# Performance work log

Measured on AMD Instinct MI355X. Metric: run time of the kernel, lower is better.

The kernel has to match this reference:

```python
import jax, jax.numpy as jnp
import numpy as np

B, N, D = 4, 2048, 512
H, DH = 8, 64
MLP = 2048
EPS = 1e-5


def setup_inputs() -> dict:
    key = jax.random.key(0)
    ks = jax.random.split(key, 8)
    s = lambda fan_in: 1.0 / np.sqrt(fan_in)
    return {
        "x": jax.random.normal(ks[0], (B, N, D), jnp.float32),
        "ln1_g": jnp.ones((D,), jnp.float32),
        "ln1_b": jnp.zeros((D,), jnp.float32),
        "Wqkv": jax.random.normal(ks[1], (D, 3 * H * DH), jnp.float32) * s(D),
        "temperature": jnp.asarray(np.log(DH ** -0.5), jnp.float32),
        "Wo": jax.random.normal(ks[2], (H * DH, D), jnp.float32) * s(H * DH),
        "bo": jnp.zeros((D,), jnp.float32),
        "ln2_g": jnp.ones((D,), jnp.float32),
        "ln2_b": jnp.zeros((D,), jnp.float32),
        "W1": jax.random.normal(ks[3], (D, MLP), jnp.float32) * s(D),
        "b1": jnp.zeros((MLP,), jnp.float32),
        "W2": jax.random.normal(ks[4], (MLP, D), jnp.float32) * s(MLP),
        "b2": jnp.zeros((D,), jnp.float32),
    }


def _layernorm(x, g, b):
    mu = jnp.mean(x, axis=-1, keepdims=True)
    var = jnp.var(x, axis=-1, keepdims=True)
    return (x - mu) * jax.lax.rsqrt(var + EPS) * g + b


def _lsa(x, Wqkv, temperature, Wo, bo):
    b, n, _ = x.shape
    qkv = x @ Wqkv  # [b, n, 3*H*DH]
    q, k, v = jnp.split(qkv, 3, axis=-1)
    rs = lambda t: t.reshape(b, n, H, DH).transpose(0, 2, 1, 3)  # b h n d
    q, k, v = rs(q), rs(k), rs(v)
    dots = jnp.einsum("bhnd,bhmd->bhnm", q, k) * jnp.exp(temperature)
    mask_value = -jnp.finfo(dots.dtype).max
    eye = jnp.eye(n, dtype=bool)
    dots = jnp.where(eye, mask_value, dots)  # mask diagonal (LSA)
    attn = jax.nn.softmax(dots, axis=-1)
    out = jnp.einsum("bhnm,bhmd->bhnd", attn, v)
    out = out.transpose(0, 2, 1, 3).reshape(b, n, H * DH)
    return out @ Wo + bo


def _ffn(x, W1, b1, W2, b2):
    h = jax.nn.gelu(x @ W1 + b1, approximate=False)
    return h @ W2 + b2


def reference(x, ln1_g, ln1_b, Wqkv, temperature, Wo, bo,
              ln2_g, ln2_b, W1, b1, W2, b2):
    y = _lsa(_layernorm(x, ln1_g, ln1_b), Wqkv, temperature, Wo, bo) + x
    z = _ffn(_layernorm(y, ln2_g, ln2_b), W1, b1, W2, b2) + y
    return (z, x)
```

## Files before the change

### kernel.cpp

```cpp
#include <hip/hip_runtime.h>
#include <math.h>

typedef __attribute__((ext_vector_type(4))) float f32x4;
typedef __attribute__((ext_vector_type(8))) short short8;

#define DEV __device__ __forceinline__

DEV short f2bf(float f){
  union { float f; unsigned u; } v; v.f = f;
  unsigned r = v.u + 0x7fffu + ((v.u >> 16) & 1u);
  return (short)(r >> 16);
}
DEV float bf2f(short s){
  union { unsigned u; float f; } v; v.u = ((unsigned)(unsigned short)s) << 16; return v.f;
}
DEV float exp2_hw(float x){ float r; asm("v_exp_f32 %0, %1" : "=v"(r) : "v"(x)); return r; }
DEV float rcp_hw(float x){ float r; asm("v_rcp_f32 %0, %1" : "=v"(r) : "v"(x)); return r; }
DEV unsigned cvtpk(float a, float b){
  unsigned r; asm("v_cvt_pk_bf16_f32 %0, %1, %2" : "=v"(r) : "v"(a), "v"(b)); return r;
}
DEV void gload_lds16(const short* src, short* lds){
  __builtin_amdgcn_global_load_lds(
      (const __attribute__((address_space(1))) void*)src,
      (__attribute__((address_space(3))) void*)lds, 16, 0, 0);
}

__global__ __launch_bounds__(256) void transpose_bf16_kernel(
    const float* __restrict__ W, short* __restrict__ Wt, int K, int N)
{
  __shared__ float tile[32][33];
  int nb = blockIdx.x * 32, kb = blockIdx.y * 32;
  int tx = threadIdx.x & 31, ty = threadIdx.x >> 5;
  #pragma unroll
  for (int i = ty; i < 32; i += 8)
    tile[i][tx] = W[(size_t)(kb + i) * N + nb + tx];
  __syncthreads();
  #pragma unroll
  for (int i = ty; i < 32; i += 8)
    Wt[(size_t)(nb + i) * K + kb + tx] = f2bf(tile[tx][i]);
}

template<int COPYX>
__global__ __launch_bounds__(256) void ln_kernel(
    const float* __restrict__ x, const float* __restrict__ g,
    const float* __restrict__ b, short* __restrict__ out,
    float* __restrict__ xcopy)
{
  int row  = blockIdx.x * 4 + (threadIdx.x >> 6);
  int lane = threadIdx.x & 63;
  const float* xr = x + (size_t)row * 512 + lane * 8;
  f32x4 v0 = *(const f32x4*)(xr);
  f32x4 v1 = *(const f32x4*)(xr + 4);
  float s  = (v0[0]+v0[1]+v0[2]+v0[3]) + (v1[0]+v1[1]+v1[2]+v1[3]);
  float sq = (v0[0]*v0[0]+v0[1]*v0[1]+v0[2]*v0[2]+v0[3]*v0[3])
           + (v1[0]*v1[0]+v1[1]*v1[1]+v1[2]*v1[2]+v1[3]*v1[3]);
  #pragma unroll
  for (int off = 1; off < 64; off <<= 1) {
    s  += __shfl_xor(s, off);
    sq += __shfl_xor(sq, off);
  }
  float mu  = s * (1.0f / 512.0f);
  float var = sq * (1.0f / 512.0f) - mu * mu;
  float rstd = rsqrtf(var + 1e-5f);
  f32x4 g0 = *(const f32x4*)(g + lane * 8);
  f32x4 g1 = *(const f32x4*)(g + lane * 8 + 4);
  f32x4 b0 = *(const f32x4*)(b + lane * 8);
  f32x4 b1 = *(const f32x4*)(b + lane * 8 + 4);
  float o[8];
  #pragma unroll
  for (int j = 0; j < 4; ++j) o[j]     = (v0[j] - mu) * rstd * g0[j] + b0[j];
  #pragma unroll
  for (int j = 0; j < 4; ++j) o[4 + j] = (v1[j] - mu) * rstd * g1[j] + b1[j];
  uint4 pk;
  pk.x = cvtpk(o[0], o[1]); pk.y = cvtpk(o[2], o[3]);
  pk.z = cvtpk(o[4], o[5]); pk.w = cvtpk(o[6], o[7]);
  *(uint4*)(out + (size_t)row * 512 + lane * 8) = pk;
  if (COPYX) {
    float* xc = xcopy + (size_t)row * 512 + lane * 8;
    *(f32x4*)(xc)     = v0;
    *(f32x4*)(xc + 4) = v1;
  }
}

template<int EPI, int BM, typename OutT>
__global__ __launch_bounds__(256) void gemm_bt_kernel(
    const short* __restrict__ A, const short* __restrict__ Bt,
    OutT* __restrict__ C, const float* __restrict__ bias,
    const float* __restrict__ resid, short* __restrict__ vt,
    int M, int N, int K)
{
  constexpr int MFR  = BM / 32;
  constexpr int NFR  = 4;
  constexpr int HALF = BM * 64 + 128 * 64;
  __shared__ __align__(16) short smem[2 * HALF];

  int tid = threadIdx.x;
  int lane = tid & 63, wid = tid >> 6;
  int l16 = lane & 15, lq = lane >> 4;

  int gx = gridDim.x;
  int nwg = gx * gridDim.y;
  int orig = blockIdx.y * gx + blockIdx.x;
  int swz = (orig & 7) * (nwg >> 3) + (orig >> 3);
  int bn = swz % gx, bm = swz / gx;

  int wm = wid >> 1, wn = wid & 1;

  const short* gaP[BM / 32];
  const short* gbP[4];
  #pragma unroll
  for (int i = 0; i < BM / 32; ++i) {
    int gg = i * 4 + wid;
    gaP[i] = A + (size_t)(bm * BM + (gg >> 1) * 16 + l16) * K + (gg & 1) * 32 + lq * 8;
  }
  #pragma unroll
  for (int i = 0; i < 4; ++i) {
    int gg = i * 4 + wid;
    gbP[i] = Bt + (size_t)(bn * 128 + (gg >> 1) * 16 + l16) * K + (gg & 1) * 32 + lq * 8;
  }

  auto STAGE = [&](int bufi, int k0) {
    short* As_ = smem + bufi * HALF;
    short* Bs_ = As_ + BM * 64;
    #pragma unroll
    for (int i = 0; i < BM / 32; ++i)
      gload_lds16(gaP[i] + k0, As_ + (i * 4 + wid) * 512);
    #pragma unroll
    for (int i = 0; i < 4; ++i)
      gload_lds16(gbP[i] + k0, Bs_ + (i * 4 + wid) * 512);
  };

  f32x4 acc[MFR][NFR] = {};

  STAGE(0, 0);
  asm volatile("s_waitcnt vmcnt(0)");
  __syncthreads();

  int nt = K >> 6;
  for (int t = 0; t < nt; ++t) {
    int cur = t & 1;
    if (t + 1 < nt) STAGE(cur ^ 1, (t + 1) << 6);
    const short* As_ = smem + cur * HALF;
    const short* Bs_ = As_ + BM * 64;
    #pragma unroll
    for (int kc = 0; kc < 2; ++kc) {
      short8 af[MFR], bfr[NFR];
      #pragma unroll
      for (int m = 0; m < MFR; ++m)
        af[m] = *(const short8*)(As_ + ((wm * MFR + m) * 2 + kc) * 512 + lane * 8);
      #pragma unroll
      for (int n = 0; n < NFR; ++n)
        bfr[n] = *(const short8*)(Bs_ + ((wn * NFR + n) * 2 + kc) * 512 + lane * 8);
      #pragma unroll
      for (int m = 0; m < MFR; ++m)
        #pragma unroll
        for (int n = 0; n < NFR; ++n)
          acc[m][n] = __builtin_amdgcn_mfma_f32_16x16x32_bf16(af[m], bfr[n], acc[m][n], 0, 0, 0);
    }
    __syncthreads();
  }

  if (EPI == 3 && bn >= 8) {
    short* T = smem;
    #pragma unroll
    for (int m = 0; m < MFR; ++m)
      #pragma unroll
      for (int n = 0; n < NFR; ++n) {
        int c = wn * 64 + n * 16 + l16;
        #pragma unroll
        for (int r = 0; r < 4; ++r) {
          int rowl = wm * 64 + m * 16 + lq * 4 + r;
          T[c * 128 + (rowl ^ ((c & 7) << 4))] = f2bf(acc[m][n][r]);
        }
      }
    __syncthreads();
    int b2 = bm >> 4;
    int nnb = (bm & 15) * 128;
    int tn = tid & 15;
    #pragma unroll
    for (int c8 = 0; c8 < 8; ++c8) {
      int c = c8 * 16 + (tid >> 4);
      short8 v = *(const short8*)(T + c * 128 + ((tn * 8) ^ ((c & 7) << 4)));
      if (tn & 1) {
        short8 w;
        #pragma unroll
        for (int j = 0; j < 8; ++j) w[j] = v[j ^ 4];
        v = w;
      }
      int c2 = bn * 128 + c - 1024;
      int bh = b2 * 8 + (c2 >> 6);
      int d  = c2 & 63;
      *(short8*)(vt + ((size_t)(bh * 64 + d)) * 2048 + nnb + tn * 8) = v;
    }
    return;
  }

  float bv[NFR];
  #pragma unroll
  for (int n = 0; n < NFR; ++n)
    bv[n] = (EPI == 0 || EPI == 3) ? 0.0f : bias[bn * 128 + (wn * NFR + n) * 16 + l16];

  #pragma unroll
  for (int m = 0; m < MFR; ++m) {
    #pragma unroll
    for (int r = 0; r < 4; ++r) {
      int row = bm * BM + (wm * MFR + m) * 16 + lq * 4 + r;
      #pragma unroll
      for (int n = 0; n < NFR; ++n) {
        int col = bn * 128 + (wn * NFR + n) * 16 + l16;
        float v = acc[m][n][r];
        if (EPI == 1 || EPI == 2) v += bv[n];
        if (EPI == 2) v = 0.5f * v * (1.0f + erff(v * 0.70710678f));
        if (EPI == 1) v += resid[(size_t)row * N + col];
        if constexpr (sizeof(OutT) == 2)
          ((short*)C)[(size_t)row * N + col] = f2bf(v);
        else
          ((float*)C)[(size_t)row * N + col] = v;
      }
    }
  }
}

__global__ __launch_bounds__(256, 2) void attn_kernel(
    const short* __restrict__ qkv, const short* __restrict__ vt,
    const float* __restrict__ temp_ptr, short* __restrict__ out)
{
  __shared__ __align__(16) short smem[16384];

  int tid = threadIdx.x;
  int lane = tid & 63, wid = tid >> 6;
  int l16 = lane & 15, lq = lane >> 4;
  int hi = lq >> 1, lq0 = lq & 1;

  int orig = blockIdx.y * 16 + blockIdx.x;
  int swz = (orig & 7) * 64 + (orig >> 3);
  int qb = swz & 15, bh = swz >> 4;
  int b = bh >> 3, h = bh & 7;

  const short* qbase = qkv + (size_t)b * 2048 * 1536 + h * 64;
  const short* kbase = qbase + 512;
  const short* vbase = vt + (size_t)bh * 64 * 2048;

  float scale = __expf(temp_ptr[0]) * 1.44269504f;
  int q0 = qb * 128 + wid * 32;

  short8 qfrag[2][2];
  #pragma unroll
  for (int qf = 0; qf < 2; ++qf) {
    int qrow = q0 + qf * 16 + l16;
    #pragma unroll
    for (int c = 0; c < 2; ++c) {
      short8 raw = *(const short8*)(qbase + (size_t)qrow * 1536 + c * 32 + lq * 8);
      short8 sc;
      #pragma unroll
      for (int j = 0; j < 8; ++j) sc[j] = f2bf(bf2f(raw[j]) * scale);
      qfrag[qf][c] = sc;
    }
  }

  f32x4 accO[2][4] = {};
  float l[2] = {0.f, 0.f};

  auto STAGE = [&](int bufi, int k0) {
    #pragma unroll
    for (int i = 0; i < 2; ++i) {
      int w16 = i * 256 + tid;
      int sub = w16 >> 7;
      int cc  = (w16 >> 6) & 1;
      int lq2 = (w16 >> 4) & 3;
      int l2  = w16 & 15;
      const short* srcK = kbase + (size_t)(k0 + sub * 16 + l2) * 1536 + cc * 32 + lq2 * 8;
      __builtin_amdgcn_global_load_lds(
          (const __attribute__((address_space(1))) void*)srcK,
          (__attribute__((address_space(3))) void*)((char*)smem + bufi * 8192 + (i * 4 + wid) * 1024),
          16, 0, 0);
      const short* srcV = vbase + (size_t)(sub * 16 + l2) * 2048 + k0 + cc * 32 + lq2 * 8;
      __builtin_amdgcn_global_load_lds(
          (const __attribute__((address_space(1))) void*)srcV,
          (__attribute__((address_space(3))) void*)((char*)smem + 16384 + bufi * 8192 + (i * 4 + wid) * 1024),
          16, 0, 0);
    }
  };

  STAGE(0, 0);
  asm volatile("s_waitcnt vmcnt(0)");
  __syncthreads();

  for (int k0 = 0; k0 < 2048; k0 += 64) {
    int cur = (k0 >> 6) & 1;
    if (k0 + 64 < 2048) STAGE(cur ^ 1, k0 + 64);

    const short* kls = smem + cur * 4096;
    const short* vls = smem + 8192 + cur * 4096;

    f32x4 accS[2][4] = {};
    __builtin_amdgcn_s_setprio(1);
    #pragma unroll
    for (int s = 0; s < 4; ++s) {
      short8 kf0 = *(const short8*)(kls + (s * 2 + 0) * 512 + lane * 8);
      short8 kf1 = *(const short8*)(kls + (s * 2 + 1) * 512 + lane * 8);
      #pragma unroll
      for (int qf = 0; qf < 2; ++qf) {
        accS[qf][s] = __builtin_amdgcn_mfma_f32_16x16x32_bf16(kf0, qfrag[qf][0], accS[qf][s], 0, 0, 0);
        accS[qf][s] = __builtin_amdgcn_mfma_f32_16x16x32_bf16(kf1, qfrag[qf][1], accS[qf][s], 0, 0, 0);
      }
    }
    __builtin_amdgcn_s_setprio(0);

    if ((q0 & ~63) == k0) {
      #pragma unroll
      for (int qf = 0; qf < 2; ++qf) {
        int qg = q0 + qf * 16 + l16;
        #pragma unroll
        for (int s = 0; s < 4; ++s)
          #pragma unroll
          for (int r = 0; r < 4; ++r)
            if (k0 + s * 16 + lq * 4 + r == qg) accS[qf][s][r] = -30000.f;
      }
    }

    short8 pa[2][2];
    #pragma unroll
    for (int qf = 0; qf < 2; ++qf) {
      float sum = 0.f;
      unsigned W[4][2];
      #pragma unroll
      for (int s = 0; s < 4; ++s) {
        float p0 = exp2_hw(accS[qf][s][0]);
        float p1 = exp2_hw(accS[qf][s][1]);
        float p2 = exp2_hw(accS[qf][s][2]);
        float p3 = exp2_hw(accS[qf][s][3]);
        sum += (p0 + p1) + (p2 + p3);
        W[s][0] = cvtpk(p0, p1);
        W[s][1] = cvtpk(p2, p3);
      }
      sum += __shfl_xor(sum, 16);
      sum += __shfl_xor(sum, 32);
      l[qf] += sum;

      unsigned K0[2], S0[2], K2[2], S2[2], R0[2], R2[2];
      #pragma unroll
      for (int w = 0; w < 2; ++w) {
        K0[w] = hi ? W[1][w] : W[0][w];
        S0[w] = hi ? W[0][w] : W[1][w];
        K2[w] = hi ? W[3][w] : W[2][w];
        S2[w] = hi ? W[2][w] : W[3][w];
      }
      #pragma unroll
      for (int w = 0; w < 2; ++w) {
        R0[w] = (unsigned)__shfl_xor((int)S0[w], 32);
        R2[w] = (unsigned)__shfl_xor((int)S2[w], 32);
      }
      bool sw = (hi != lq0);
      unsigned FA[2], FB[2], sA[2], sB[2], GA[2], GB[2];
      #pragma unroll
      for (int w = 0; w < 2; ++w) {
        sA[w] = sw ? K0[w] : R0[w];  FA[w] = sw ? R0[w] : K0[w];
        sB[w] = sw ? K2[w] : R2[w];  FB[w] = sw ? R2[w] : K2[w];
      }
      #pragma unroll
      for (int w = 0; w < 2; ++w) {
        GA[w] = (unsigned)__shfl_xor((int)sA[w], 16);
        GB[w] = (unsigned)__shfl_xor((int)sB[w], 16);
      }
      union { unsigned u[4]; short8 s8; } p0u, p1u;
      p0u.u[0] = FA[0]; p0u.u[1] = FA[1]; p0u.u[2] = GA[0]; p0u.u[3] = GA[1];
      p1u.u[0] = FB[0]; p1u.u[1] = FB[1]; p1u.u[2] = GB[0]; p1u.u[3] = GB[1];
      pa[qf][0] = p0u.s8;
      pa[qf][1] = p1u.s8;
    }

    short8 vfr[4][2];
    #pragma unroll
    for (int d = 0; d < 4; ++d) {
      vfr[d][0] = *(const short8*)(vls + (d * 2 + 0) * 512 + lane * 8);
      vfr[d][1] = *(const short8*)(vls + (d * 2 + 1) * 512 + lane * 8);
    }
    __builtin_amdgcn_s_setprio(1);
    #pragma unroll
    for (int qf = 0; qf < 2; ++qf)
      #pragma unroll
      for (int d = 0; d < 4; ++d) {
        accO[qf][d] = __builtin_amdgcn_mfma_f32_16x16x32_bf16(vfr[d][0], pa[qf][0], accO[qf][d], 0, 0, 0);
        accO[qf][d] = __builtin_amdgcn_mfma_f32_16x16x32_bf16(vfr[d][1], pa[qf][1], accO[qf][d], 0, 0, 0);
      }
    __builtin_amdgcn_s_setprio(0);

    __syncthreads();
  }

  #pragma unroll
  for (int qf = 0; qf < 2; ++qf) {
    float inv = rcp_hw(l[qf]);
    int qg = q0 + qf * 16 + l16;
    size_t rowoff = (size_t)(b * 2048 + qg) * 512 + h * 64;
    #pragma unroll
    for (int d = 0; d < 4; ++d) {
      unsigned w0 = cvtpk(accO[qf][d][0] * inv, accO[qf][d][1] * inv);
      unsigned w1 = cvtpk(accO[qf][d][2] * inv, accO[qf][d][3] * inv);
      uint2 pk; pk.x = w0; pk.y = w1;
      *(uint2*)(out + rowoff + d * 16 + lq * 4) = pk;
    }
  }
}

extern "C" void kernel_launch(void* const* d_in, const int* in_sizes, int n_in,
                              void* d_out, int out_size, void* d_ws, size_t ws_size,
                              hipStream_t stream)
{
  const float* x    = (const float*)d_in[0];
  const float* ln1g = (const float*)d_in[1];
  const float* ln1b = (const float*)d_in[2];
  const float* Wqkv = (const float*)d_in[3];
  const float* temp = (const float*)d_in[4];
  const float* Wo   = (const float*)d_in[5];
  const float* bo   = (const float*)d_in[6];
  const float* ln2g = (const float*)d_in[7];
  const float* ln2b = (const float*)d_in[8];
  const float* W1   = (const float*)d_in[9];
  const float* b1   = (const float*)d_in[10];
  const float* W2   = (const float*)d_in[11];
  const float* b2   = (const float*)d_in[12];
  float* out = (float*)d_out;

  char* ws = (char*)d_ws;
  short* wqkv_t = (short*)(ws);
  short* wo_t   = (short*)(ws + 1572864);
  short* w1_t   = (short*)(ws + 2097152);
  short* w2_t   = (short*)(ws + 4194304);
  short* h      = (short*)(ws + 6291456);
  short* qkv    = (short*)(ws + 14680064);
  short* attn   = (short*)(ws + 39845888);
  float* y      = (float*)(ws + 48234496);
  short* vt     = (short*)(ws + 48234496);
  short* t      = (short*)(ws + 14680064);

  const int M = 8192;

  transpose_bf16_kernel<<<dim3(1536 / 32, 512 / 32),  256, 0, stream>>>(Wqkv, wqkv_t, 512, 1536);
  transpose_bf16_kernel<<<dim3(512 / 32, 512 / 32),   256, 0, stream>>>(Wo,   wo_t,   512, 512);
  transpose_bf16_kernel<<<dim3(2048 / 32, 512 / 32),  256, 0, stream>>>(W1,   w1_t,   512, 2048);
  transpose_bf16_kernel<<<dim3(512 / 32, 2048 / 32),  256, 0, stream>>>(W2,   w2_t,   2048, 512);

  ln_kernel<1><<<M / 4, 256, 0, stream>>>(x, ln1g, ln1b, h, out + (size_t)M * 512);

  gemm_bt_kernel<3, 128, short><<<dim3(1536 / 128, M / 128), 256, 0, stream>>>(
      h, wqkv_t, qkv, nullptr, nullptr, vt, M, 1536, 512);

  attn_kernel<<<dim3(16, 32), 256, 0, stream>>>(qkv, vt, temp, attn);

  gemm_bt_kernel<1, 64, float><<<dim3(512 / 128, M / 64), 256, 0, stream>>>(
      attn, wo_t, y, bo, x, nullptr, M, 512, 512);

  ln_kernel<0><<<M / 4, 256, 0, stream>>>(y, ln2g, ln2b, h, nullptr);

  gemm_bt_kernel<2, 128, short><<<dim3(2048 / 128, M / 128), 256, 0, stream>>>(
      h, w1_t, t, b1, nullptr, nullptr, M, 2048, 512);

  gemm_bt_kernel<1, 64, float><<<dim3(512 / 128, M / 64), 256, 0, stream>>>(
      t, w2_t, out, b2, y, nullptr, M, 512, 2048);
}
```

Baseline: 232.6 us.

## Triple-buffer LDS staging in GEMM and attention with partial vmcnt waits

Both the GEMM and the attention kernel move from double-buffered LDS staging with a full vmcnt(0) wait plus two barriers per iteration to a three-stage ring buffer. Each iteration waits only on the oldest outstanding load group and issues a single barrier. The GEMM k-step also shrinks from 64 to 32, so each stage holds a smaller tile, and MFMA blocks get raised priority. The goal is to keep two global-to-LDS loads in flight and hide memory latency behind compute. In exchange the attention kernel uses more LDS, which can limit occupancy, and the hand-counted vmcnt values must match the exact number of loads issued per stage.

```diff
diff --git a/kernel.cpp b/kernel.cpp
--- a/kernel.cpp
+++ b/kernel.cpp
@@ -89,10 +89,11 @@
     const float* __restrict__ resid, short* __restrict__ vt,
     int M, int N, int K)
 {
-  constexpr int MFR  = BM / 32;
-  constexpr int NFR  = 4;
-  constexpr int HALF = BM * 64 + 128 * 64;
-  __shared__ __align__(16) short smem[2 * HALF];
+  constexpr int MFR = BM / 32;
+  constexpr int NFR = 4;
+  constexpr int AI  = BM / 64;
+  constexpr int BUF = BM * 32 + 128 * 32;
+  __shared__ __align__(16) short smem[3 * BUF];
 
   int tid = threadIdx.x;
   int lane = tid & 63, wid = tid >> 6;
@@ -106,61 +107,65 @@
 
   int wm = wid >> 1, wn = wid & 1;
 
-  const short* gaP[BM / 32];
-  const short* gbP[4];
-  #pragma unroll
-  for (int i = 0; i < BM / 32; ++i) {
+  const short* gaP[AI];
+  const short* gbP[2];
+  #pragma unroll
+  for (int i = 0; i < AI; ++i) {
     int gg = i * 4 + wid;
-    gaP[i] = A + (size_t)(bm * BM + (gg >> 1) * 16 + l16) * K + (gg & 1) * 32 + lq * 8;
-  }
-  #pragma unroll
-  for (int i = 0; i < 4; ++i) {
+    gaP[i] = A + (size_t)(bm * BM + gg * 16 + l16) * K + lq * 8;
+  }
+  #pragma unroll
+  for (int i = 0; i < 2; ++i) {
     int gg = i * 4 + wid;
-    gbP[i] = Bt + (size_t)(bn * 128 + (gg >> 1) * 16 + l16) * K + (gg & 1) * 32 + lq * 8;
+    gbP[i] = Bt + (size_t)(bn * 128 + gg * 16 + l16) * K + lq * 8;
   }
 
   auto STAGE = [&](int bufi, int k0) {
-    short* As_ = smem + bufi * HALF;
-    short* Bs_ = As_ + BM * 64;
-    #pragma unroll
-    for (int i = 0; i < BM / 32; ++i)
-      gload_lds16(gaP[i] + k0, As_ + (i * 4 + wid) * 512);
-    #pragma unroll
-    for (int i = 0; i < 4; ++i)
-      gload_lds16(gbP[i] + k0, Bs_ + (i * 4 + wid) * 512);
+    short* base = smem + bufi * BUF;
+    #pragma unroll
+    for (int i = 0; i < AI; ++i)
+      gload_lds16(gaP[i] + k0, base + (i * 4 + wid) * 512);
+    #pragma unroll
+    for (int i = 0; i < 2; ++i)
+      gload_lds16(gbP[i] + k0, base + BM * 32 + (i * 4 + wid) * 512);
   };
 
   f32x4 acc[MFR][NFR] = {};
 
   STAGE(0, 0);
-  asm volatile("s_waitcnt vmcnt(0)");
-  __syncthreads();
-
-  int nt = K >> 6;
+  STAGE(1, 32);
+
+  int nt = K >> 5;
   for (int t = 0; t < nt; ++t) {
-    int cur = t & 1;
-    if (t + 1 < nt) STAGE(cur ^ 1, (t + 1) << 6);
-    const short* As_ = smem + cur * HALF;
-    const short* Bs_ = As_ + BM * 64;
-    #pragma unroll
-    for (int kc = 0; kc < 2; ++kc) {
-      short8 af[MFR], bfr[NFR];
-      #pragma unroll
-      for (int m = 0; m < MFR; ++m)
-        af[m] = *(const short8*)(As_ + ((wm * MFR + m) * 2 + kc) * 512 + lane * 8);
+    if (t + 1 < nt) {
+      if constexpr (AI == 2) asm volatile("s_waitcnt vmcnt(4)" ::: "memory");
+      else                   asm volatile("s_waitcnt vmcnt(3)" ::: "memory");
+    } else {
+      asm volatile("s_waitcnt vmcnt(0)" ::: "memory");
+    }
+    __builtin_amdgcn_s_barrier();
+    __builtin_amdgcn_sched_barrier(0);
+    if (t + 2 < nt) STAGE((t + 2) % 3, (t + 2) << 5);
+
+    const short* base = smem + (t % 3) * BUF;
+    short8 af[MFR], bfr[NFR];
+    #pragma unroll
+    for (int m = 0; m < MFR; ++m)
+      af[m] = *(const short8*)(base + (wm * MFR + m) * 512 + lane * 8);
+    #pragma unroll
+    for (int n = 0; n < NFR; ++n)
+      bfr[n] = *(const short8*)(base + BM * 32 + (wn * NFR + n) * 512 + lane * 8);
+    __builtin_amdgcn_s_setprio(1);
+    #pragma unroll
+    for (int m = 0; m < MFR; ++m)
       #pragma unroll
       for (int n = 0; n < NFR; ++n)
-        bfr[n] = *(const short8*)(Bs_ + ((wn * NFR + n) * 2 + kc) * 512 + lane * 8);
-      #pragma unroll
-      for (int m = 0; m < MFR; ++m)
-        #pragma unroll
-        for (int n = 0; n < NFR; ++n)
-          acc[m][n] = __builtin_amdgcn_mfma_f32_16x16x32_bf16(af[m], bfr[n], acc[m][n], 0, 0, 0);
-    }
+        acc[m][n] = __builtin_amdgcn_mfma_f32_16x16x32_bf16(af[m], bfr[n], acc[m][n], 0, 0, 0);
+    __builtin_amdgcn_s_setprio(0);
+  }
+
+  if (EPI == 3 && bn >= 8) {
     __syncthreads();
-  }
-
-  if (EPI == 3 && bn >= 8) {
     short* T = smem;
     #pragma unroll
     for (int m = 0; m < MFR; ++m)
@@ -225,7 +230,7 @@
     const short* __restrict__ qkv, const short* __restrict__ vt,
     const float* __restrict__ temp_ptr, short* __restrict__ out)
 {
-  __shared__ __align__(16) short smem[16384];
+  __shared__ __align__(16) short smem[24576];
 
   int tid = threadIdx.x;
   int lane = tid & 63, wid = tid >> 6;
@@ -270,28 +275,25 @@
       int lq2 = (w16 >> 4) & 3;
       int l2  = w16 & 15;
       const short* srcK = kbase + (size_t)(k0 + sub * 16 + l2) * 1536 + cc * 32 + lq2 * 8;
-      __builtin_amdgcn_global_load_lds(
-          (const __attribute__((address_space(1))) void*)srcK,
-          (__attribute__((address_space(3))) void*)((char*)smem + bufi * 8192 + (i * 4 + wid) * 1024),
-          16, 0, 0);
+      gload_lds16(srcK, smem + bufi * 4096 + (i * 4 + wid) * 512);
       const short* srcV = vbase + (size_t)(sub * 16 + l2) * 2048 + k0 + cc * 32 + lq2 * 8;
-      __builtin_amdgcn_global_load_lds(
-          (const __attribute__((address_space(1))) void*)srcV,
-          (__attribute__((address_space(3))) void*)((char*)smem + 16384 + bufi * 8192 + (i * 4 + wid) * 1024),
-          16, 0, 0);
+      gload_lds16(srcV, smem + 12288 + bufi * 4096 + (i * 4 + wid) * 512);
     }
   };
 
   STAGE(0, 0);
-  asm volatile("s_waitcnt vmcnt(0)");
-  __syncthreads();
-
-  for (int k0 = 0; k0 < 2048; k0 += 64) {
-    int cur = (k0 >> 6) & 1;
-    if (k0 + 64 < 2048) STAGE(cur ^ 1, k0 + 64);
-
-    const short* kls = smem + cur * 4096;
-    const short* vls = smem + 8192 + cur * 4096;
+  STAGE(1, 64);
+
+  for (int t = 0; t < 32; ++t) {
+    if (t + 1 < 32) asm volatile("s_waitcnt vmcnt(4)" ::: "memory");
+    else            asm volatile("s_waitcnt vmcnt(0)" ::: "memory");
+    __builtin_amdgcn_s_barrier();
+    __builtin_amdgcn_sched_barrier(0);
+    if (t + 2 < 32) STAGE((t + 2) % 3, (t + 2) * 64);
+
+    int k0 = t * 64;
+    const short* kls = smem + (t % 3) * 4096;
+    const short* vls = smem + 12288 + (t % 3) * 4096;
 
     f32x4 accS[2][4] = {};
     __builtin_amdgcn_s_setprio(1);
@@ -385,8 +387,6 @@
         accO[qf][d] = __builtin_amdgcn_mfma_f32_16x16x32_bf16(vfr[d][1], pa[qf][1], accO[qf][d], 0, 0, 0);
       }
     __builtin_amdgcn_s_setprio(0);
-
-    __syncthreads();
   }
 
   #pragma unroll
```

Result: faster. 223.9 us (-3.7%).
